# Optimization experiments

Measured on AMD Instinct MI355X. Metric: run time of the kernel, lower is better.

The kernel has to match this reference:

```python
import jax, jax.numpy as jnp
import numpy as np

N_ROUTES = 7      # len(ROUTES): 3 unimodal + 3 bimodal + 1 trimodal routes
PC_DIM = 512      # primary capsule pose dim
MC_DIM = 128      # output (decision) capsule pose dim
K = 25            # num_classes (phenotypes)
NUM_ROUTING = 3   # routing iterations
B = 4096


def _layer_norm(x, gamma, beta, eps=1e-5):
    mu = jnp.mean(x, axis=-1, keepdims=True)
    var = jnp.var(x, axis=-1, keepdims=True)
    return (x - mu) * jax.lax.rsqrt(var + eps) * gamma + beta


def setup_inputs() -> dict:
    key = jax.random.key(0)
    ks = jax.random.split(key, 4)
    w_std = float(np.sqrt(K / (PC_DIM * N_ROUTES)))  # CapsuleFC weight init scale
    return {
        "prim_pose": jax.random.normal(ks[0], (B, N_ROUTES, PC_DIM), dtype=jnp.float32),
        "prim_act": jax.random.uniform(ks[1], (B, N_ROUTES), dtype=jnp.float32),
        "w": w_std * jax.random.normal(ks[2], (N_ROUTES, PC_DIM, K, MC_DIM), dtype=jnp.float32),
        "ln_gamma": jnp.ones((MC_DIM,), dtype=jnp.float32),
        "ln_beta": jnp.zeros((MC_DIM,), dtype=jnp.float32),
        "embedding": 0.02 * jax.random.normal(ks[3], (K, MC_DIM), dtype=jnp.float32),
        "bias": jnp.zeros((K,), dtype=jnp.float32),
    }


def reference(prim_pose, prim_act, w, ln_gamma, ln_beta, embedding, bias):
    # prim_pose: [B, N, D_in]; prim_act: [B, N]
    act = prim_act[..., None]                      # [B, N, 1]
    scale = 1.0 / np.sqrt(MC_DIM)
    # Votes are constant across routing iterations; hoist out of the loop.
    vote = jnp.einsum('bnd,ndmv->bnmv', prim_pose, w)  # [B, N, K, Dv]
    next_pose = None
    routing_coef = None
    for it in range(NUM_ROUTING):
        if next_pose is None:
            # iteration 0: uniform routing coefficients (softmax of zeros over out capsules)
            routing_coef = jnp.full((prim_pose.shape[0], N_ROUTES, K), 1.0 / K,
                                    dtype=prim_pose.dtype)
        else:
            # inverted dot-product attention: agreement between votes and current decision pose
            agree = jnp.einsum('bnmv,bmv->bnm', vote, next_pose) * scale
            routing_coef = jax.nn.softmax(agree, axis=-1)
        c = routing_coef * act                     # weight routing by primary activations
        next_pose = _layer_norm(jnp.einsum('bnm,bnmv->bmv', c, vote), ln_gamma, ln_beta)
        # act_type='ONES' -> decision activations are all ones (no effect on routing)
    logits = jnp.einsum('bmd,md->bm', next_pose, embedding) + bias  # [B, K]
    return logits, prim_act, routing_coef
```

## Files before the change

kernel.cpp:

```cpp
#include <hip/hip_runtime.h>
#include <hip/hip_bf16.h>
#include <math.h>

#define N_ROUTES 7
#define PC_DIM   512
#define MC_DIM   128
#define KCLS     25
#define BATCH    4096

#define ROW_IN   (N_ROUTES * PC_DIM)
#define JDIM     (KCLS * MC_DIM)
#define VOTE_B   (N_ROUTES * JDIM)

typedef __attribute__((ext_vector_type(8))) _Float16 half8;
typedef __attribute__((ext_vector_type(4))) float f32x4;

__device__ inline ushort f2h(float f) {
    _Float16 h = (_Float16)f;
    return __builtin_bit_cast(ushort, h);
}

__device__ inline float2 h2f2(uint u) {
    union { uint x; _Float16 h[2]; } c; c.x = u;
    return make_float2((float)c.h[0], (float)c.h[1]);
}

__device__ inline void load_lds16(const void* g, void* l) {
    __builtin_amdgcn_global_load_lds(
        (const __attribute__((address_space(1))) void*)g,
        (__attribute__((address_space(3))) void*)l, 16, 0, 0);
}

__global__ __launch_bounds__(256) void conv_pose(const float* __restrict__ p,
                                                 ushort* __restrict__ pb, int n8) {
    int i = blockIdx.x * 256 + threadIdx.x;
    if (i >= n8) return;
    const float4* s = (const float4*)p + (size_t)i * 2;
    float4 a = s[0], b = s[1];
    ushort t[8];
    t[0]=f2h(a.x); t[1]=f2h(a.y); t[2]=f2h(a.z); t[3]=f2h(a.w);
    t[4]=f2h(b.x); t[5]=f2h(b.y); t[6]=f2h(b.z); t[7]=f2h(b.w);
    *(uint4*)(pb + (size_t)i * 8) = *(uint4*)t;
}

__global__ __launch_bounds__(256) void conv_w(const float* __restrict__ w,
                                              ushort* __restrict__ wt) {
    __shared__ float t[32][65];
    const int j0 = blockIdx.x * 32, d0 = blockIdx.y * 64, r = blockIdx.z;
    const int jc = threadIdx.x & 31, dr0 = threadIdx.x >> 5;
    const float* wp = w + (size_t)r * PC_DIM * JDIM;
#pragma unroll
    for (int i = 0; i < 8; i++)
        t[jc][dr0 + i * 8] = wp[(size_t)(d0 + dr0 + i * 8) * JDIM + j0 + jc];
    __syncthreads();
    const int jr = threadIdx.x >> 3, dc = (threadIdx.x & 7) * 8;
    ushort o[8];
#pragma unroll
    for (int k = 0; k < 8; k++) o[k] = f2h(t[jr][dc + k]);
    ushort* op = wt + (size_t)r * JDIM * PC_DIM;
    *(uint4*)(op + (size_t)(j0 + jr) * PC_DIM + d0 + dc) = *(uint4*)o;
}


#define BAR() do { __builtin_amdgcn_sched_barrier(0); \
                   __builtin_amdgcn_s_barrier(); \
                   __builtin_amdgcn_sched_barrier(0); } while (0)
#define WAIT_VM(n) do { asm volatile("s_waitcnt vmcnt(" #n ")" ::: "memory"); } while (0)

__global__ __launch_bounds__(256, 2) void vote_gemm_mfma(
        const ushort* __restrict__ poseb,
        const ushort* __restrict__ wt,
        ushort* __restrict__ vote,
        int rows) {
    __shared__ __align__(16) char smem[73728];

    int route, rowTile, jTile;
    {
        const int blk = blockIdx.x;
        if (gridDim.x == 2800) {
            const int x = blk & 7;
            const int g = blk >> 3;
            const int q = g / 25;
            jTile = g - q * 25;
            const int p = x * 14 + q;
            route = p >> 4;
            rowTile = p & 15;
        } else {
            rowTile = blk / 175;
            const int rem = blk - rowTile * 175;
            route = rem / 25;
            jTile = rem - route * 25;
        }
    }
    const int b0 = rowTile * 256;
    const int j0 = jTile * 128;

    const int tid = threadIdx.x;
    const int l = tid & 63, w = tid >> 6;
    const int wm = w >> 1, wn = w & 1;
    const int lm = l & 15, q4 = l >> 4;
    const int xr = (l >> 1) & 3;

    const ushort* Aptr = poseb + (size_t)route * PC_DIM;
    const ushort* Bptr = wt + (size_t)route * JDIM * PC_DIM;

    uint aof[4], bof[2];
    {
#pragma unroll
        for (int i = 0; i < 4; i++) {
            const int f = tid + i * 256;
            const int row = f >> 2, c = f & 3;
            const int qg = c ^ ((row >> 1) & 3);
            int ga = b0 + row; if (ga >= rows) ga = rows - 1;
            aof[i] = (uint)ga * ROW_IN + qg * 8;
        }
#pragma unroll
        for (int i = 0; i < 2; i++) {
            const int f = tid + i * 256;
            const int row = f >> 2, c = f & 3;
            const int qg = c ^ ((row >> 1) & 3);
            bof[i] = (uint)(j0 + row) * PC_DIM + qg * 8;
        }
    }

    const int aBase = ((wm * 128 + lm) * 4 + (q4 ^ xr)) * 16;
    const int bBase = 16384 + ((wn * 64 + lm) * 4 + (q4 ^ xr)) * 16;

    f32x4 acc[8][4] = {};

#define STAGE(kt) do { \
        char* d_ = smem + (((kt) % 3) * 24576); \
        load_lds16(Aptr + aof[0] + (kt) * 32, d_ + (size_t)tid * 16); \
        load_lds16(Aptr + aof[1] + (kt) * 32, d_ + (size_t)(tid + 256) * 16); \
        load_lds16(Aptr + aof[2] + (kt) * 32, d_ + (size_t)(tid + 512) * 16); \
        load_lds16(Aptr + aof[3] + (kt) * 32, d_ + (size_t)(tid + 768) * 16); \
        load_lds16(Bptr + bof[0] + (kt) * 32, d_ + 16384 + (size_t)tid * 16); \
        load_lds16(Bptr + bof[1] + (kt) * 32, d_ + 16384 + (size_t)(tid + 256) * 16); \
    } while (0)

    STAGE(0); STAGE(1);
    WAIT_VM(6);
    BAR();

#pragma unroll
    for (int t = 0; t < 16; ++t) {
        if (t < 14) STAGE(t + 2);
        const char* bp_ = smem + ((t % 3) * 24576);
        half8 af[8], bf[4];
#pragma unroll
        for (int nt = 0; nt < 4; nt++)
            bf[nt] = *(const half8*)(bp_ + bBase + nt * 1024);
#pragma unroll
        for (int mt = 0; mt < 8; mt++)
            af[mt] = *(const half8*)(bp_ + aBase + mt * 1024);
#pragma unroll
        for (int mt = 0; mt < 8; mt++)
#pragma unroll
            for (int nt = 0; nt < 4; nt++)
                acc[mt][nt] = __builtin_amdgcn_mfma_f32_16x16x32_f16(
                    af[mt], bf[nt], acc[mt][nt], 0, 0, 0);
        if (t < 14)       WAIT_VM(6);
        else if (t == 14) WAIT_VM(0);
        BAR();
    }

    const int erow = l >> 2, ec0 = (l & 3) * 16;
#pragma unroll
    for (int mt = 0; mt < 8; mt++) {
        float* ep = (float*)smem + w * 1088 + (mt & 1) * 4352;
#pragma unroll
        for (int nt = 0; nt < 4; nt++)
#pragma unroll
            for (int i = 0; i < 4; i++)
                ep[(q4 * 4 + i) * 68 + nt * 16 + lm] = acc[mt][nt][i];
        asm volatile("s_waitcnt lgkmcnt(0)" ::: "memory");
        const int grow = b0 + wm * 128 + mt * 16 + erow;
        if (grow < rows) {
            ushort t16[16];
#pragma unroll
            for (int t8 = 0; t8 < 4; t8++) {
                float4 v = *(float4*)&ep[erow * 68 + ec0 + t8 * 4];
                t16[t8*4+0]=f2h(v.x); t16[t8*4+1]=f2h(v.y);
                t16[t8*4+2]=f2h(v.z); t16[t8*4+3]=f2h(v.w);
            }
            ushort* dst = vote + (size_t)grow * VOTE_B + route * JDIM + j0 + wn * 64 + ec0;
            ((uint4*)dst)[0] = ((uint4*)t16)[0];
            ((uint4*)dst)[1] = ((uint4*)t16)[1];
        }
    }
}

__global__ __launch_bounds__(448) void routing_kernel(
        const ushort* __restrict__ vote16,
        const float* __restrict__ act,
        const float* __restrict__ gamma,
        const float* __restrict__ beta,
        const float* __restrict__ emb,
        const float* __restrict__ bias,
        float* __restrict__ out_logits,
        float* __restrict__ out_act,
        float* __restrict__ out_coef) {
    const int b = blockIdx.x;
    __shared__ float coef_s[N_ROUTES * KCLS];
    __shared__ float act_s[8];

    const int tid = threadIdx.x, l = tid & 63, wv = tid >> 6;
    const int sub = l & 15, mg = l >> 4;
    const int m = wv + 7 * mg;
    const bool mv = (m < KCLS);

    if (tid < N_ROUTES) {
        float a = act[(size_t)b * N_ROUTES + tid];
        act_s[tid] = a;
        out_act[(size_t)b * N_ROUTES + tid] = a;
    }

    float vf[N_ROUTES][8];
    if (mv) {
        const uint4* vb = (const uint4*)(vote16 + (size_t)b * VOTE_B);
#pragma unroll
        for (int n = 0; n < N_ROUTES; n++) {
            uint4 q = vb[n * 400 + m * 16 + sub];
            float2 f0 = h2f2(q.x), f1 = h2f2(q.y), f2 = h2f2(q.z), f3 = h2f2(q.w);
            vf[n][0] = f0.x; vf[n][1] = f0.y; vf[n][2] = f1.x; vf[n][3] = f1.y;
            vf[n][4] = f2.x; vf[n][5] = f2.y; vf[n][6] = f3.x; vf[n][7] = f3.y;
        }
    } else {
#pragma unroll
        for (int n = 0; n < N_ROUTES; n++)
#pragma unroll
            for (int j = 0; j < 8; j++) vf[n][j] = 0.f;
    }
    const int mc = mv ? m : 24;

    float g[8], be[8];
    *(float4*)(g)      = *(const float4*)(gamma + 8 * sub);
    *(float4*)(g + 4)  = *(const float4*)(gamma + 8 * sub + 4);
    *(float4*)(be)     = *(const float4*)(beta  + 8 * sub);
    *(float4*)(be + 4) = *(const float4*)(beta  + 8 * sub + 4);
    __syncthreads();

    const float scale = 0.088388347648318447f;
    float pose[8];

    auto update = [&](bool first) {
        float r[8];
#pragma unroll
        for (int j = 0; j < 8; j++) r[j] = 0.f;
#pragma unroll
        for (int n = 0; n < N_ROUTES; n++) {
            float c = first ? (act_s[n] * 0.04f) : (coef_s[n * KCLS + mc] * act_s[n]);
#pragma unroll
            for (int j = 0; j < 8; j++) r[j] += c * vf[n][j];
        }
        float S = 0.f, Q = 0.f;
#pragma unroll
        for (int j = 0; j < 8; j++) { S += r[j]; Q += r[j] * r[j]; }
#pragma unroll
        for (int o = 8; o; o >>= 1) {
            S += __shfl_xor(S, o);
            Q += __shfl_xor(Q, o);
        }
        float mean = S * 0.0078125f;
        float var  = Q * 0.0078125f - mean * mean;
        float rs   = rsqrtf(var + 1e-5f);
#pragma unroll
        for (int j = 0; j < 8; j++) pose[j] = (r[j] - mean) * rs * g[j] + be[j];
    };

    update(true);
    __syncthreads();

    const int sgrp = tid >> 5, slane = tid & 31;

    for (int it = 1; it < 3; it++) {
        float d[N_ROUTES];
#pragma unroll
        for (int n = 0; n < N_ROUTES; n++) {
            float t = 0.f;
#pragma unroll
            for (int j = 0; j < 8; j++) t += vf[n][j] * pose[j];
            d[n] = t;
        }
#pragma unroll
        for (int o = 8; o; o >>= 1)
#pragma unroll
            for (int n = 0; n < N_ROUTES; n++) d[n] += __shfl_xor(d[n], o);
        if (sub == 0 && mv) {
#pragma unroll
            for (int n = 0; n < N_ROUTES; n++) coef_s[n * KCLS + m] = d[n] * scale;
        }
        __syncthreads();
        if (sgrp < N_ROUTES) {
            float c = (slane < KCLS) ? coef_s[sgrp * KCLS + slane] : -1e30f;
            float mx = c;
#pragma unroll
            for (int o = 16; o; o >>= 1) mx = fmaxf(mx, __shfl_xor(mx, o, 32));
            float e = (slane < KCLS) ? expf(c - mx) : 0.f;
            float s = e;
#pragma unroll
            for (int o = 16; o; o >>= 1) s += __shfl_xor(s, o, 32);
            if (slane < KCLS) coef_s[sgrp * KCLS + slane] = e / s;
        }
        __syncthreads();
        update(false);
        if (it == 1) __syncthreads();
    }

    float e[8];
    *(float4*)(e)     = *(const float4*)(emb + mc * MC_DIM + 8 * sub);
    *(float4*)(e + 4) = *(const float4*)(emb + mc * MC_DIM + 8 * sub + 4);
    float dd = 0.f;
#pragma unroll
    for (int j = 0; j < 8; j++) dd += pose[j] * e[j];
#pragma unroll
    for (int o = 8; o; o >>= 1) dd += __shfl_xor(dd, o);
    if (sub == 0 && mv) out_logits[(size_t)b * KCLS + m] = dd + bias[m];

    if (tid < N_ROUTES * KCLS)
        out_coef[(size_t)b * (N_ROUTES * KCLS) + tid] = coef_s[tid];
}

extern "C" void kernel_launch(void* const* d_in, const int* in_sizes, int n_in,
                              void* d_out, int out_size, void* d_ws, size_t ws_size,
                              hipStream_t stream) {
    const float* pose  = (const float*)d_in[0];
    const float* act   = (const float*)d_in[1];
    const float* w     = (const float*)d_in[2];
    const float* gamma = (const float*)d_in[3];
    const float* beta  = (const float*)d_in[4];
    const float* emb   = (const float*)d_in[5];
    const float* bias  = (const float*)d_in[6];

    float* out        = (float*)d_out;
    float* out_logits = out;
    float* out_act    = out + BATCH * KCLS;
    float* out_coef   = out + BATCH * KCLS + BATCH * N_ROUTES;

    const size_t wt_bytes    = (size_t)N_ROUTES * JDIM * PC_DIM * 2;
    const size_t poseb_bytes = (size_t)BATCH * ROW_IN * 2;
    ushort* wt    = (ushort*)d_ws;
    ushort* poseb = (ushort*)((char*)d_ws + wt_bytes);
    ushort* voteh = (ushort*)((char*)d_ws + wt_bytes + poseb_bytes);

    size_t rem = ws_size > wt_bytes + poseb_bytes ? ws_size - wt_bytes - poseb_bytes : 0;
    size_t cap = rem / ((size_t)VOTE_B * 2);
    int chunk;
    if (cap >= (size_t)BATCH)  chunk = BATCH;
    else if (cap >= 256)       chunk = (int)(cap & ~(size_t)255);
    else                       chunk = (int)(cap > 0 ? cap : 1);

    conv_w<<<dim3(JDIM / 32, PC_DIM / 64, N_ROUTES), 256, 0, stream>>>(w, wt);
    const int n8 = BATCH * ROW_IN / 8;
    conv_pose<<<(n8 + 255) / 256, 256, 0, stream>>>(pose, poseb, n8);

    for (int b0 = 0; b0 < BATCH; b0 += chunk) {
        int rows = BATCH - b0 < chunk ? BATCH - b0 : chunk;
        int nRowTiles = (rows + 255) / 256;
        vote_gemm_mfma<<<nRowTiles * 175, 256, 0, stream>>>(
            poseb + (size_t)b0 * ROW_IN, wt, voteh, rows);
        routing_kernel<<<rows, 448, 0, stream>>>(
            voteh,
            act + (size_t)b0 * N_ROUTES,
            gamma, beta, emb, bias,
            out_logits + (size_t)b0 * KCLS,
            out_act    + (size_t)b0 * N_ROUTES,
            out_coef   + (size_t)b0 * N_ROUTES * KCLS);
    }
}
```

Measured before the change: 320.0 us.

## Fuse vote GEMM and routing into one kernel to overlap batch halves

Merges the vote GEMM and routing kernels into one launchable kernel whose blocks act as either GEMM tiles or routing rows, depending on block index. The batch is split in half: the second launch runs the GEMM for the second half while routing the first half, so the memory-bound routing can overlap the MFMA-bound GEMM. Because both roles share a 448-thread block, the GEMM blocks leave 192 threads idle, spinning through matching barriers. The launch-bounds change (448 threads, 4 blocks per CU) may raise register pressure or lower occupancy for the GEMM path.

New measurement: 1.106 ms. 245% more time.

```diff
diff --git a/kernel.cpp b/kernel.cpp
--- a/kernel.cpp
+++ b/kernel.cpp
@@ -66,67 +66,86 @@
                    __builtin_amdgcn_s_barrier(); \
                    __builtin_amdgcn_sched_barrier(0); } while (0)
 #define WAIT_VM(n) do { asm volatile("s_waitcnt vmcnt(" #n ")" ::: "memory"); } while (0)
-
-__global__ __launch_bounds__(256, 2) void vote_gemm_mfma(
+#define GEMM_BARRIERS 17
+
+__global__ __launch_bounds__(448, 4) void gemm_route(
         const ushort* __restrict__ poseb,
         const ushort* __restrict__ wt,
         ushort* __restrict__ vote,
-        int rows) {
+        int nG, int gRow0, int gRows, int vRow0,
+        const float* __restrict__ act,
+        const float* __restrict__ gamma,
+        const float* __restrict__ beta,
+        const float* __restrict__ emb,
+        const float* __restrict__ bias,
+        float* __restrict__ out_logits,
+        float* __restrict__ out_act,
+        float* __restrict__ out_coef,
+        int rRow0) {
     __shared__ __align__(16) char smem[73728];
-
-    int route, rowTile, jTile;
-    {
-        const int blk = blockIdx.x;
-        if (gridDim.x == 2800) {
-            const int x = blk & 7;
-            const int g = blk >> 3;
-            const int q = g / 25;
-            jTile = g - q * 25;
-            const int p = x * 14 + q;
-            route = p >> 4;
-            rowTile = p & 15;
-        } else {
-            rowTile = blk / 175;
-            const int rem = blk - rowTile * 175;
-            route = rem / 25;
-            jTile = rem - route * 25;
-        }
-    }
-    const int b0 = rowTile * 256;
-    const int j0 = jTile * 128;
-
-    const int tid = threadIdx.x;
-    const int l = tid & 63, w = tid >> 6;
-    const int wm = w >> 1, wn = w & 1;
-    const int lm = l & 15, q4 = l >> 4;
-    const int xr = (l >> 1) & 3;
-
-    const ushort* Aptr = poseb + (size_t)route * PC_DIM;
-    const ushort* Bptr = wt + (size_t)route * JDIM * PC_DIM;
-
-    uint aof[4], bof[2];
-    {
-#pragma unroll
-        for (int i = 0; i < 4; i++) {
-            const int f = tid + i * 256;
-            const int row = f >> 2, c = f & 3;
-            const int qg = c ^ ((row >> 1) & 3);
-            int ga = b0 + row; if (ga >= rows) ga = rows - 1;
-            aof[i] = (uint)ga * ROW_IN + qg * 8;
-        }
-#pragma unroll
-        for (int i = 0; i < 2; i++) {
-            const int f = tid + i * 256;
-            const int row = f >> 2, c = f & 3;
-            const int qg = c ^ ((row >> 1) & 3);
-            bof[i] = (uint)(j0 + row) * PC_DIM + qg * 8;
-        }
-    }
-
-    const int aBase = ((wm * 128 + lm) * 4 + (q4 ^ xr)) * 16;
-    const int bBase = 16384 + ((wn * 64 + lm) * 4 + (q4 ^ xr)) * 16;
-
-    f32x4 acc[8][4] = {};
+    __shared__ float coef_s[N_ROUTES * KCLS];
+    __shared__ float act_s[8];
+
+    if ((int)blockIdx.x < nG) {
+        const int tid = threadIdx.x;
+        if (tid >= 256) {
+            for (int i = 0; i < GEMM_BARRIERS; i++) __builtin_amdgcn_s_barrier();
+            return;
+        }
+        int route, rowTile, jTile;
+        {
+            const int blk = blockIdx.x;
+            if (nG == 1400 && gRows == 2048) {
+                const int x = blk & 7;
+                const int g = blk >> 3;
+                const int q = g / 25;
+                jTile = g - q * 25;
+                const int p = x * 7 + q;
+                route = p >> 3;
+                rowTile = (p & 7) + (gRow0 >> 8);
+            } else {
+                const int rtl = blk / 175;
+                const int rem = blk - rtl * 175;
+                route = rem / 25;
+                jTile = rem - route * 25;
+                rowTile = rtl + (gRow0 >> 8);
+            }
+        }
+        const int b0 = rowTile * 256;
+        const int j0 = jTile * 128;
+        const int lastRow = gRow0 + gRows - 1;
+
+        const int l = tid & 63, w = tid >> 6;
+        const int wm = w >> 1, wn = w & 1;
+        const int lm = l & 15, q4 = l >> 4;
+        const int xr = (l >> 1) & 3;
+
+        const ushort* Aptr = poseb + (size_t)route * PC_DIM;
+        const ushort* Bptr = wt + (size_t)route * JDIM * PC_DIM;
+
+        uint aof[4], bof[2];
+        {
+#pragma unroll
+            for (int i = 0; i < 4; i++) {
+                const int f = tid + i * 256;
+                const int row = f >> 2, c = f & 3;
+                const int qg = c ^ ((row >> 1) & 3);
+                int ga = b0 + row; if (ga > lastRow) ga = lastRow;
+                aof[i] = (uint)ga * ROW_IN + qg * 8;
+            }
+#pragma unroll
+            for (int i = 0; i < 2; i++) {
+                const int f = tid + i * 256;
+                const int row = f >> 2, c = f & 3;
+                const int qg = c ^ ((row >> 1) & 3);
+                bof[i] = (uint)(j0 + row) * PC_DIM + qg * 8;
+            }
+        }
+
+        const int aBase = ((wm * 128 + lm) * 4 + (q4 ^ xr)) * 16;
+        const int bBase = 16384 + ((wn * 64 + lm) * 4 + (q4 ^ xr)) * 16;
+
+        f32x4 acc[8][4] = {};
 
 #define STAGE(kt) do { \
         char* d_ = smem + (((kt) % 3) * 24576); \
@@ -138,71 +157,63 @@
         load_lds16(Bptr + bof[1] + (kt) * 32, d_ + 16384 + (size_t)(tid + 256) * 16); \
     } while (0)
 
-    STAGE(0); STAGE(1);
-    WAIT_VM(6);
-    BAR();
-
-#pragma unroll
-    for (int t = 0; t < 16; ++t) {
-        if (t < 14) STAGE(t + 2);
-        const char* bp_ = smem + ((t % 3) * 24576);
-        half8 af[8], bf[4];
-#pragma unroll
-        for (int nt = 0; nt < 4; nt++)
-            bf[nt] = *(const half8*)(bp_ + bBase + nt * 1024);
-#pragma unroll
-        for (int mt = 0; mt < 8; mt++)
-            af[mt] = *(const half8*)(bp_ + aBase + mt * 1024);
-#pragma unroll
-        for (int mt = 0; mt < 8; mt++)
+        STAGE(0); STAGE(1);
+        WAIT_VM(6);
+        BAR();
+
+#pragma unroll
+        for (int t = 0; t < 16; ++t) {
+            if (t < 14) STAGE(t + 2);
+            const char* bp_ = smem + ((t % 3) * 24576);
+            half8 af[8], bf[4];
 #pragma unroll
             for (int nt = 0; nt < 4; nt++)
-                acc[mt][nt] = __builtin_amdgcn_mfma_f32_16x16x32_f16(
-                    af[mt], bf[nt], acc[mt][nt], 0, 0, 0);
-        if (t < 14)       WAIT_VM(6);
-        else if (t == 14) WAIT_VM(0);
-        BAR();
-    }
-
-    const int erow = l >> 2, ec0 = (l & 3) * 16;
-#pragma unroll
-    for (int mt = 0; mt < 8; mt++) {
-        float* ep = (float*)smem + w * 1088 + (mt & 1) * 4352;
-#pragma unroll
-        for (int nt = 0; nt < 4; nt++)
-#pragma unroll
-            for (int i = 0; i < 4; i++)
-                ep[(q4 * 4 + i) * 68 + nt * 16 + lm] = acc[mt][nt][i];
-        asm volatile("s_waitcnt lgkmcnt(0)" ::: "memory");
-        const int grow = b0 + wm * 128 + mt * 16 + erow;
-        if (grow < rows) {
-            ushort t16[16];
-#pragma unroll
-            for (int t8 = 0; t8 < 4; t8++) {
-                float4 v = *(float4*)&ep[erow * 68 + ec0 + t8 * 4];
-                t16[t8*4+0]=f2h(v.x); t16[t8*4+1]=f2h(v.y);
-                t16[t8*4+2]=f2h(v.z); t16[t8*4+3]=f2h(v.w);
+                bf[nt] = *(const half8*)(bp_ + bBase + nt * 1024);
+#pragma unroll
+            for (int mt = 0; mt < 8; mt++)
+                af[mt] = *(const half8*)(bp_ + aBase + mt * 1024);
+#pragma unroll
+            for (int mt = 0; mt < 8; mt++)
+#pragma unroll
+                for (int nt = 0; nt < 4; nt++)
+                    acc[mt][nt] = __builtin_amdgcn_mfma_f32_16x16x32_f16(
+                        af[mt], bf[nt], acc[mt][nt], 0, 0, 0);
+            if (t < 14)       WAIT_VM(6);
+            else if (t == 14) WAIT_VM(0);
+            BAR();
+        }
+
+        const int erow = l >> 2, ec0 = (l & 3) * 16;
+#pragma unroll
+        for (int mt = 0; mt < 8; mt++) {
+            float* ep = (float*)smem + w * 1088 + (mt & 1) * 4352;
+#pragma unroll
+            for (int nt = 0; nt < 4; nt++)
+#pragma unroll
+                for (int i = 0; i < 4; i++)
+                    ep[(q4 * 4 + i) * 68 + nt * 16 + lm] = acc[mt][nt][i];
+            asm volatile("s_waitcnt lgkmcnt(0)" ::: "memory");
+            const int grow = b0 + wm * 128 + mt * 16 + erow;
+            if (grow <= lastRow) {
+                ushort t16[16];
+#pragma unroll
+                for (int t8 = 0; t8 < 4; t8++) {
+                    float4 v = *(float4*)&ep[erow * 68 + ec0 + t8 * 4];
+                    t16[t8*4+0]=f2h(v.x); t16[t8*4+1]=f2h(v.y);
+                    t16[t8*4+2]=f2h(v.z); t16[t8*4+3]=f2h(v.w);
+                }
+                ushort* dst = vote + (size_t)(grow - vRow0) * VOTE_B
+                                   + route * JDIM + j0 + wn * 64 + ec0;
+                ((uint4*)dst)[0] = ((uint4*)t16)[0];
+                ((uint4*)dst)[1] = ((uint4*)t16)[1];
             }
-            ushort* dst = vote + (size_t)grow * VOTE_B + route * JDIM + j0 + wn * 64 + ec0;
-            ((uint4*)dst)[0] = ((uint4*)t16)[0];
-            ((uint4*)dst)[1] = ((uint4*)t16)[1];
-        }
-    }
-}
-
-__global__ __launch_bounds__(448) void routing_kernel(
-        const ushort* __restrict__ vote16,
-        const float* __restrict__ act,
-        const float* __restrict__ gamma,
-        const float* __restrict__ beta,
-        const float* __restrict__ emb,
-        const float* __restrict__ bias,
-        float* __restrict__ out_logits,
-        float* __restrict__ out_act,
-        float* __restrict__ out_coef) {
-    const int b = blockIdx.x;
-    __shared__ float coef_s[N_ROUTES * KCLS];
-    __shared__ float act_s[8];
+        }
+#undef STAGE
+        return;
+    }
+
+    const int b = rRow0 + ((int)blockIdx.x - nG);
+    const ushort* vote16 = vote + (size_t)(b - vRow0) * VOTE_B;
 
     const int tid = threadIdx.x, l = tid & 63, wv = tid >> 6;
     const int sub = l & 15, mg = l >> 4;
@@ -217,7 +228,7 @@
 
     float vf[N_ROUTES][8];
     if (mv) {
-        const uint4* vb = (const uint4*)(vote16 + (size_t)b * VOTE_B);
+        const uint4* vb = (const uint4*)vote16;
 #pragma unroll
         for (int n = 0; n < N_ROUTES; n++) {
             uint4 q = vb[n * 400 + m * 16 + sub];
@@ -345,26 +356,35 @@
 
     size_t rem = ws_size > wt_bytes + poseb_bytes ? ws_size - wt_bytes - poseb_bytes : 0;
     size_t cap = rem / ((size_t)VOTE_B * 2);
-    int chunk;
-    if (cap >= (size_t)BATCH)  chunk = BATCH;
-    else if (cap >= 256)       chunk = (int)(cap & ~(size_t)255);
-    else                       chunk = (int)(cap > 0 ? cap : 1);
 
     conv_w<<<dim3(JDIM / 32, PC_DIM / 64, N_ROUTES), 256, 0, stream>>>(w, wt);
     const int n8 = BATCH * ROW_IN / 8;
     conv_pose<<<(n8 + 255) / 256, 256, 0, stream>>>(pose, poseb, n8);
 
-    for (int b0 = 0; b0 < BATCH; b0 += chunk) {
-        int rows = BATCH - b0 < chunk ? BATCH - b0 : chunk;
-        int nRowTiles = (rows + 255) / 256;
-        vote_gemm_mfma<<<nRowTiles * 175, 256, 0, stream>>>(
-            poseb + (size_t)b0 * ROW_IN, wt, voteh, rows);
-        routing_kernel<<<rows, 448, 0, stream>>>(
-            voteh,
-            act + (size_t)b0 * N_ROUTES,
-            gamma, beta, emb, bias,
-            out_logits + (size_t)b0 * KCLS,
-            out_act    + (size_t)b0 * N_ROUTES,
-            out_coef   + (size_t)b0 * N_ROUTES * KCLS);
-    }
-}
+    if (cap >= (size_t)BATCH) {
+        const int H = BATCH / 2;
+        gemm_route<<<1400, 448, 0, stream>>>(
+            poseb, wt, voteh, 1400, 0, H, 0,
+            act, gamma, beta, emb, bias, out_logits, out_act, out_coef, 0);
+        gemm_route<<<1400 + H, 448, 0, stream>>>(
+            poseb, wt, voteh, 1400, H, H, 0,
+            act, gamma, beta, emb, bias, out_logits, out_act, out_coef, 0);
+        gemm_route<<<H, 448, 0, stream>>>(
+            poseb, wt, voteh, 0, 0, 0, 0,
+            act, gamma, beta, emb, bias, out_logits, out_act, out_coef, H);
+    } else {
+        int chunk;
+        if (cap >= 256) chunk = (int)(cap & ~(size_t)255);
+        else            chunk = (int)(cap > 0 ? cap : 1);
+        for (int b0 = 0; b0 < BATCH; b0 += chunk) {
+            int rows = BATCH - b0 < chunk ? BATCH - b0 : chunk;
+            int nRT = (rows + 255) / 256;
+            gemm_route<<<nRT * 175, 448, 0, stream>>>(
+                poseb, wt, voteh, nRT * 175, b0, rows, b0,
+                act, gamma, beta, emb, bias, out_logits, out_act, out_coef, 0);
+            gemm_route<<<rows, 448, 0, stream>>>(
+                poseb, wt, voteh, 0, 0, 0, b0,
+                act, gamma, beta, emb, bias, out_logits, out_act, out_coef, b0);
+        }
+    }
+}
```
